# Kernel optimization log

Measured on AMD Instinct MI355X. Metric: run time of the kernel, lower is better.

The kernel has to match this reference:

```python
import jax, jax.numpy as jnp
import numpy as np

EMBED = 1024
HEADS = 16
HEAD_DIM = EMBED // HEADS


def setup_inputs() -> dict:
    key = jax.random.key(0)
    ks = jax.random.split(key, 12)
    B, S = 2, 2048
    inp = {
        'v': jax.random.normal(ks[0], (B, S, EMBED), jnp.float32),
        'k': jax.random.normal(ks[1], (B, S, EMBED), jnp.float32),
        'q': jax.random.normal(ks[2], (B, S, EMBED), jnp.float32),
        'mask': jnp.ones((B, 1, S, S), dtype=bool),
        'Wv': jax.random.normal(ks[3], (EMBED, EMBED), jnp.float32) * 0.02,
        'bv': jax.random.normal(ks[4], (EMBED,), jnp.float32) * 0.02,
        'Wk': jax.random.normal(ks[5], (EMBED, EMBED), jnp.float32) * 0.02,
        'bk': jax.random.normal(ks[6], (EMBED,), jnp.float32) * 0.02,
        'Wq': jax.random.normal(ks[7], (EMBED, EMBED), jnp.float32) * 0.02,
        'bq': jax.random.normal(ks[8], (EMBED,), jnp.float32) * 0.02,
        'Wo': jax.random.normal(ks[9], (EMBED, EMBED), jnp.float32) * 0.02,
        'bo': jax.random.normal(ks[10], (EMBED,), jnp.float32) * 0.02,
    }
    return inp


def reference(v, k, q, mask, Wv, bv, Wk, bk, Wq, bq, Wo, bo):
    N, q_len, _ = q.shape
    k_len = k.shape[1]
    # linear projections (torch Linear: x @ W.T + b)
    vh = (v @ Wv.T + bv).reshape(N, -1, HEADS, HEAD_DIM)
    kh = (k @ Wk.T + bk).reshape(N, k_len, HEADS, HEAD_DIM)
    qh = (q @ Wq.T + bq).reshape(N, q_len, HEADS, HEAD_DIM)
    # scores [N, H, q, k]
    energy = jnp.einsum('nqhd,nkhd->nhqk', qh, kh)
    # NOTE: original masks BEFORE dividing by sqrt(embed_size)
    energy = jnp.where(mask, energy, jnp.float32(-1e20))
    attention = jax.nn.softmax(energy / jnp.sqrt(jnp.float32(EMBED)), axis=3)
    out = jnp.einsum('nhqk,nkhd->nqhd', attention, vh).reshape(N, q_len, EMBED)
    return out @ Wo.T + bo
```

## Files before the change

### kernel.cpp

```cpp
#include <hip/hip_runtime.h>
#include <cstdint>
#include <cstddef>


typedef uint16_t u16;
typedef uint32_t u32;
typedef unsigned long long u64;
using bf16x8 = __attribute__((ext_vector_type(8))) __bf16;
using bf16x2 = __attribute__((ext_vector_type(2))) __bf16;
using f32x4  = __attribute__((ext_vector_type(4))) float;
using f32x16 = __attribute__((ext_vector_type(16))) float;
using u16x8  = __attribute__((ext_vector_type(8))) uint16_t;
using u16x4  = __attribute__((ext_vector_type(4))) uint16_t;
using u32x4  = __attribute__((ext_vector_type(4))) uint32_t;

#define S_LEN 2048
#define EMB   1024
#define NHEAD 16
#define HDIM  64
#define BATCH 2
#define MROWS (BATCH * S_LEN)
#define NBITW (BATCH * S_LEN * (S_LEN / 64))

__device__ __forceinline__ u16 f2bf(float f) {
  uint32_t u = __float_as_uint(f);
  u += 0x7FFFu + ((u >> 16) & 1u);
  return (u16)(u >> 16);
}

__device__ __forceinline__ float fexp2(float x) {
#if __has_builtin(__builtin_amdgcn_exp2f)
  return __builtin_amdgcn_exp2f(x);
#else
  return exp2f(x);
#endif
}

__device__ __forceinline__ u32 packbf(float a, float b) {
  bf16x2 v = { (__bf16)a, (__bf16)b };
  return __builtin_bit_cast(u32, v);
}

__device__ __forceinline__ void plswap(u32& a, u32& b) {
  asm volatile("v_permlane32_swap_b32 %0, %1" : "+v"(a), "+v"(b));
}

__device__ __forceinline__ void async16(void* lds, const void* g) {
  __builtin_amdgcn_global_load_lds(
      (const __attribute__((address_space(1))) void*)g,
      (__attribute__((address_space(3))) void*)lds, 16, 0, 0);
}

__global__ __launch_bounds__(256) void mask_compact(const uint32_t* __restrict__ m,
                                                    u64* __restrict__ bits) {
  const int i = blockIdx.x * 256 + threadIdx.x;
  if (i >= NBITW) return;
  const bool bytew = (m[0] == 0x01010101u);
  u64 b = 0;
  if (bytew) {
    const uint32_t* src = m + (size_t)i * 16;
#pragma unroll
    for (int w = 0; w < 16; ++w) {
      const uint32_t v = src[w];
#pragma unroll
      for (int j = 0; j < 4; ++j)
        b |= (u64)(((v >> (8 * j)) & 0xFFu) != 0u) << (w * 4 + j);
    }
  } else {
    const uint32_t* src = m + (size_t)i * 64;
#pragma unroll
    for (int j = 0; j < 64; ++j) b |= (u64)(src[j] != 0u) << j;
  }
  bits[i] = b;
}

struct ConvArgs {
  const float* src[7];
  u16* dst[7];
  int n4[7];
};

__global__ __launch_bounds__(256) void convert_bf16(ConvArgs a) {
  const int j = blockIdx.y;
  const float4* s = (const float4*)a.src[j];
  u16* d = a.dst[j];
  const int n4 = a.n4[j];
  for (int i = blockIdx.x * 256 + threadIdx.x; i < n4; i += gridDim.x * 256) {
    float4 v = s[i];
    u16x4 o = { f2bf(v.x), f2bf(v.y), f2bf(v.z), f2bf(v.w) };
    *(u16x4*)(d + (size_t)i * 4) = o;
  }
}

template <int BM, int BN, int FM, int FN, typename OutT>
__device__ __forceinline__ void gemm_body(const u16* __restrict__ A,
                                          const u16* __restrict__ W,
                                          const float* __restrict__ bias,
                                          OutT* __restrict__ C, float scale) {
  constexpr int K = 1024, N = 1024;
  __shared__ alignas(16) u16 As[BM * 32];
  __shared__ alignas(16) u16 Bs[BN * 32];
  const int t = threadIdx.x;
  const int wave = t >> 6, lane = t & 63;
  const int wr = wave >> 1, wc = wave & 1;
  const int m0 = blockIdx.y * BM, n0 = blockIdx.x * BN;
  f32x4 acc[FM][FN] = {};
  const int srow = wave * 16 + (lane >> 2);
  const int soff = (lane & 3) * 8;
  const u16* gA = A + (size_t)(m0 + srow) * K + soff;
  const u16* gB = W + (size_t)(n0 + srow) * K + soff;
  u16* lA = As + wave * 512;
  u16* lB = Bs + wave * 512;
  const int fo = (lane >> 4) * 8;
  const int fr = lane & 15;

  for (int kt = 0; kt < K; kt += 32) {
#pragma unroll
    for (int a = 0; a < BM / 64; ++a)
      async16(lA + a * 2048, gA + (size_t)(a * 64) * K + kt);
#pragma unroll
    for (int a = 0; a < BN / 64; ++a)
      async16(lB + a * 2048, gB + (size_t)(a * 64) * K + kt);
    __syncthreads();
    bf16x8 af[FM], bfr[FN];
#pragma unroll
    for (int i = 0; i < FM; ++i)
      af[i] = *(const bf16x8*)(As + (wr * (FM * 16) + i * 16 + fr) * 32 + fo);
#pragma unroll
    for (int i = 0; i < FN; ++i)
      bfr[i] = *(const bf16x8*)(Bs + (wc * (FN * 16) + i * 16 + fr) * 32 + fo);
#pragma unroll
    for (int mi = 0; mi < FM; ++mi)
#pragma unroll
      for (int ni = 0; ni < FN; ++ni)
        acc[mi][ni] = __builtin_amdgcn_mfma_f32_16x16x32_bf16(af[mi], bfr[ni],
                                                              acc[mi][ni], 0, 0, 0);
    __syncthreads();
  }
  const int r0 = (lane >> 4) * 4;
#pragma unroll
  for (int mi = 0; mi < FM; ++mi) {
    const int rowb = m0 + wr * (FM * 16) + mi * 16 + r0;
#pragma unroll
    for (int ni = 0; ni < FN; ++ni) {
      const int col = n0 + wc * (FN * 16) + ni * 16 + fr;
      const float bv = bias[col];
#pragma unroll
      for (int r = 0; r < 4; ++r) {
        float v = (acc[mi][ni][r] + bv) * scale;
        if constexpr (sizeof(OutT) == 2)
          C[(size_t)(rowb + r) * N + col] = f2bf(v);
        else
          C[(size_t)(rowb + r) * N + col] = v;
      }
    }
  }
}

struct ProjArgs {
  const u16* A[3];
  const u16* W[3];
  const float* bias[3];
  u16* C[3];
  float scale[3];
};

__global__ __launch_bounds__(256) void gemm_proj3(ProjArgs p) {
  const int z = blockIdx.z;
  gemm_body<128, 128, 4, 4, u16>(p.A[z], p.W[z], p.bias[z], p.C[z], p.scale[z]);
}

__global__ __launch_bounds__(256) void gemm_out(const u16* __restrict__ A,
                                                const u16* __restrict__ W,
                                                const float* __restrict__ bias,
                                                float* __restrict__ C) {
  gemm_body<64, 128, 2, 4, float>(A, W, bias, C, 1.0f);
}

__global__ __launch_bounds__(256, 2) void attn_fa(const u16* __restrict__ Qh,
                                                  const u16* __restrict__ Kh,
                                                  const u16* __restrict__ Vh,
                                                  const u64* __restrict__ mbits,
                                                  u16* __restrict__ O) {
  __shared__ alignas(16) u16 Kt[2][64 * 64];
  __shared__ alignas(16) u16 Vt[2][64 * 64];
  const int t = threadIdx.x, wave = t >> 6, lane = t & 63;
  const int b = blockIdx.y >> 4, h = blockIdx.y & 15;
  const int ql = lane & 31;
  const int hi = lane >> 5;
  const int qrow = blockIdx.x * 128 + wave * 32 + ql;

  const u16* qbase = Qh + (size_t)(b * S_LEN + qrow) * EMB + h * HDIM + hi * 8;
  bf16x8 qf[4];
#pragma unroll
  for (int dk = 0; dk < 4; ++dk)
    qf[dk] = *(const bf16x8*)(qbase + dk * 16);

  const int srow = t >> 3;
  const int schunk = t & 7;
  const int fk0 = (srow + (srow >> 3)) & 7;
  const int fk1 = (srow + 32 + ((srow + 32) >> 3)) & 7;
  const u16* kbase = Kh + (size_t)(b * S_LEN) * EMB + h * HDIM;
  const u16* vbase = Vh + (size_t)(b * S_LEN) * EMB + h * HDIM;
  const int vdg = t & 7, vkp = t >> 3;
  const int vd0 = vdg * 8, vk0 = vkp * 2;
  const int vg_hi = (vkp >> 2) & 7, vg_lo = (vkp & 3) * 4;

  u16x8 va, vb;
  {
    async16(&Kt[0][0] + wave * 512,
            kbase + (size_t)srow * EMB + ((schunk ^ fk0) * 8));
    async16(&Kt[0][0] + 2048 + wave * 512,
            kbase + (size_t)(srow + 32) * EMB + ((schunk ^ fk1) * 8));
    const u16* vs = vbase + (size_t)vk0 * EMB + vd0;
    va = *(const u16x8*)vs;
    vb = *(const u16x8*)(vs + EMB);
  }
#pragma unroll
  for (int j = 0; j < 8; ++j) {
    const int d = vd0 + j;
    const int fd = (d + (d >> 3)) & 7;
    const u32 val = (u32)va[j] | ((u32)vb[j] << 16);
    *(u32*)((char*)&Vt[0][0] + (d * 128 + ((vg_hi ^ fd) << 4) + vg_lo)) = val;
  }
  __syncthreads();

  f32x16 o[2] = {};
  float mreg = -1.0e30f, lloc = 0.f;
  const u64* mword = mbits + (size_t)(b * S_LEN + qrow) * 32;

  for (int kt = 0; kt < 32; ++kt) {
    const int cur = kt & 1, nxt = cur ^ 1;
    if (kt < 31) {
      const int kvn = (kt + 1) * 64;
      async16(&Kt[nxt][0] + wave * 512,
              kbase + (size_t)(kvn + srow) * EMB + ((schunk ^ fk0) * 8));
      async16(&Kt[nxt][0] + 2048 + wave * 512,
              kbase + (size_t)(kvn + srow + 32) * EMB + ((schunk ^ fk1) * 8));
      const u16* vs = vbase + (size_t)(kvn + vk0) * EMB + vd0;
      va = *(const u16x8*)vs;
      vb = *(const u16x8*)(vs + EMB);
    }

    f32x16 s[2] = {};
#pragma unroll
    for (int kb = 0; kb < 2; ++kb) {
      const int key = kb * 32 + ql;
      const int fkk = (key + (key >> 3)) & 7;
      const char* kRow = (const char*)&Kt[cur][0] + key * 128;
#pragma unroll
      for (int dk = 0; dk < 4; ++dk) {
        const bf16x8 kf =
            *(const bf16x8*)(kRow + (((dk * 2 + hi) ^ fkk) << 4));
        s[kb] = __builtin_amdgcn_mfma_f32_32x32x16_bf16(kf, qf[dk], s[kb], 0, 0, 0);
      }
    }

    const u64 mw = mword[kt];
    if (!__all((int)(mw == ~0ull))) {
#pragma unroll
      for (int kb = 0; kb < 2; ++kb)
#pragma unroll
        for (int r = 0; r < 16; ++r) {
          const int key = 32 * kb + (r & 3) + 8 * (r >> 2) + 4 * hi;
          if (!((mw >> key) & 1ull)) s[kb][r] = -1.0e20f;
        }
    }

    float tm = s[0][0];
#pragma unroll
    for (int kb = 0; kb < 2; ++kb)
#pragma unroll
      for (int r = 0; r < 16; ++r) tm = fmaxf(tm, s[kb][r]);
    tm = fmaxf(tm, __shfl_xor(tm, 32));
    if (!__all((int)(tm <= mreg + 8.0f))) {
      const float mn = fmaxf(mreg, tm);
      const float al = fexp2(mreg - mn);
      mreg = mn;
      lloc *= al;
#pragma unroll
      for (int dB = 0; dB < 2; ++dB)
#pragma unroll
        for (int r = 0; r < 16; ++r) o[dB][r] *= al;
    }
    float ts = 0.f;
#pragma unroll
    for (int kb = 0; kb < 2; ++kb)
#pragma unroll
      for (int r = 0; r < 16; ++r) {
        const float p = fexp2(s[kb][r] - mreg);
        s[kb][r] = p;
        ts += p;
      }
    lloc += ts;

    bf16x8 pf[4];
#pragma unroll
    for (int kb = 0; kb < 2; ++kb) {
      u32 w0 = packbf(s[kb][0], s[kb][1]);
      u32 w1 = packbf(s[kb][2], s[kb][3]);
      u32 w2 = packbf(s[kb][4], s[kb][5]);
      u32 w3 = packbf(s[kb][6], s[kb][7]);
      u32 w4 = packbf(s[kb][8], s[kb][9]);
      u32 w5 = packbf(s[kb][10], s[kb][11]);
      u32 w6 = packbf(s[kb][12], s[kb][13]);
      u32 w7 = packbf(s[kb][14], s[kb][15]);
      plswap(w0, w2);
      plswap(w1, w3);
      plswap(w4, w6);
      plswap(w5, w7);
      const u32x4 lo = {w0, w1, w2, w3};
      const u32x4 hi4 = {w4, w5, w6, w7};
      pf[kb * 2 + 0] = __builtin_bit_cast(bf16x8, lo);
      pf[kb * 2 + 1] = __builtin_bit_cast(bf16x8, hi4);
    }

#pragma unroll
    for (int dB = 0; dB < 2; ++dB) {
      const int d = dB * 32 + ql;
      const int fd = (d + (d >> 3)) & 7;
      const char* vRow = (const char*)&Vt[cur][0] + d * 128;
#pragma unroll
      for (int ks = 0; ks < 4; ++ks) {
        const bf16x8 vf =
            *(const bf16x8*)(vRow + (((ks * 2 + hi) ^ fd) << 4));
        o[dB] = __builtin_amdgcn_mfma_f32_32x32x16_bf16(vf, pf[ks], o[dB], 0, 0, 0);
      }
    }

    if (kt < 31) {
#pragma unroll
      for (int j = 0; j < 8; ++j) {
        const int d = vd0 + j;
        const int fd = (d + (d >> 3)) & 7;
        const u32 val = (u32)va[j] | ((u32)vb[j] << 16);
        *(u32*)((char*)&Vt[nxt][0] + (d * 128 + ((vg_hi ^ fd) << 4) + vg_lo)) = val;
      }
    }
    __syncthreads();
  }

  const float inv = 1.0f / (lloc + __shfl_xor(lloc, 32));
  u16* ob = O + (size_t)(b * S_LEN + qrow) * EMB + h * HDIM;
#pragma unroll
  for (int dB = 0; dB < 2; ++dB)
#pragma unroll
    for (int rr = 0; rr < 4; ++rr) {
      u16x4 st;
#pragma unroll
      for (int m = 0; m < 4; ++m) st[m] = f2bf(o[dB][rr * 4 + m] * inv);
      *(u16x4*)(ob + dB * 32 + rr * 8 + hi * 4) = st;
    }
}

extern "C" void kernel_launch(void* const* d_in, const int* in_sizes, int n_in,
                              void* d_out, int out_size, void* d_ws, size_t ws_size,
                              hipStream_t stream) {
  const float* v_in = (const float*)d_in[0];
  const float* k_in = (const float*)d_in[1];
  const float* q_in = (const float*)d_in[2];
  const uint32_t* mask = (const uint32_t*)d_in[3];
  const float* Wv = (const float*)d_in[4];
  const float* bv = (const float*)d_in[5];
  const float* Wk = (const float*)d_in[6];
  const float* bk = (const float*)d_in[7];
  const float* Wq = (const float*)d_in[8];
  const float* bq = (const float*)d_in[9];
  const float* Wo = (const float*)d_in[10];
  const float* bo = (const float*)d_in[11];

  char* ws = (char*)d_ws;
  const size_t SZX = (size_t)MROWS * EMB * 2;
  const size_t SZW = (size_t)EMB * EMB * 2;
  u16* qh  = (u16*)(ws);
  u16* kh  = (u16*)(ws + SZX);
  u16* vh  = (u16*)(ws + 2 * SZX);
  u16* Obf = (u16*)(ws + 3 * SZX);
  u16* Wqb = (u16*)(ws + 4 * SZX);
  u16* Wkb = (u16*)(ws + 4 * SZX + SZW);
  u16* Wvb = (u16*)(ws + 4 * SZX + 2 * SZW);
  u16* Wob = (u16*)(ws + 4 * SZX + 3 * SZW);
  u16* qbf = (u16*)(ws + 4 * SZX + 4 * SZW);
  u16* kbf = (u16*)(ws + 5 * SZX + 4 * SZW);
  u16* vbf = (u16*)(ws + 6 * SZX + 4 * SZW);
  u64* mbits = (u64*)(ws + 7 * SZX + 4 * SZW);

  mask_compact<<<dim3(NBITW / 256), 256, 0, stream>>>(mask, mbits);

  ConvArgs ca;
  ca.src[0] = q_in; ca.dst[0] = qbf; ca.n4[0] = MROWS * EMB / 4;
  ca.src[1] = k_in; ca.dst[1] = kbf; ca.n4[1] = MROWS * EMB / 4;
  ca.src[2] = v_in; ca.dst[2] = vbf; ca.n4[2] = MROWS * EMB / 4;
  ca.src[3] = Wq;   ca.dst[3] = Wqb; ca.n4[3] = EMB * EMB / 4;
  ca.src[4] = Wk;   ca.dst[4] = Wkb; ca.n4[4] = EMB * EMB / 4;
  ca.src[5] = Wv;   ca.dst[5] = Wvb; ca.n4[5] = EMB * EMB / 4;
  ca.src[6] = Wo;   ca.dst[6] = Wob; ca.n4[6] = EMB * EMB / 4;
  convert_bf16<<<dim3(256, 7), 256, 0, stream>>>(ca);

  ProjArgs pa;
  const float qscale = 1.4426950408889634f / 32.0f;
  pa.A[0] = qbf; pa.W[0] = Wqb; pa.bias[0] = bq; pa.C[0] = qh; pa.scale[0] = qscale;
  pa.A[1] = kbf; pa.W[1] = Wkb; pa.bias[1] = bk; pa.C[1] = kh; pa.scale[1] = 1.0f;
  pa.A[2] = vbf; pa.W[2] = Wvb; pa.bias[2] = bv; pa.C[2] = vh; pa.scale[2] = 1.0f;
  gemm_proj3<<<dim3(8, 32, 3), 256, 0, stream>>>(pa);

  attn_fa<<<dim3(S_LEN / 128, BATCH * NHEAD), 256, 0, stream>>>(qh, kh, vh, mbits, Obf);

  gemm_out<<<dim3(8, 64), 256, 0, stream>>>(Obf, Wob, bo, (float*)d_out);
}
```

Before: 142.3 us.

## Quad-buffer K/V tiles in attention, halving barriers, with setprio and permlane reductions

```diff
diff --git a/kernel.cpp b/kernel.cpp
--- a/kernel.cpp
+++ b/kernel.cpp
@@ -43,6 +43,19 @@
 
 __device__ __forceinline__ void plswap(u32& a, u32& b) {
   asm volatile("v_permlane32_swap_b32 %0, %1" : "+v"(a), "+v"(b));
+}
+
+__device__ __forceinline__ float xhalf_max(float x) {
+  u32 a = __builtin_bit_cast(u32, x), b;
+  asm volatile("v_mov_b32 %0, %1" : "=v"(b) : "v"(a));
+  asm volatile("v_permlane32_swap_b32 %0, %1" : "+v"(a), "+v"(b));
+  return fmaxf(__builtin_bit_cast(float, a), __builtin_bit_cast(float, b));
+}
+__device__ __forceinline__ float xhalf_sum(float x) {
+  u32 a = __builtin_bit_cast(u32, x), b;
+  asm volatile("v_mov_b32 %0, %1" : "=v"(b) : "v"(a));
+  asm volatile("v_permlane32_swap_b32 %0, %1" : "+v"(a), "+v"(b));
+  return __builtin_bit_cast(float, a) + __builtin_bit_cast(float, b);
 }
 
 __device__ __forceinline__ void async16(void* lds, const void* g) {
@@ -182,8 +195,8 @@
                                                   const u16* __restrict__ Vh,
                                                   const u64* __restrict__ mbits,
                                                   u16* __restrict__ O) {
-  __shared__ alignas(16) u16 Kt[2][64 * 64];
-  __shared__ alignas(16) u16 Vt[2][64 * 64];
+  __shared__ alignas(16) u16 Kt[4][64 * 64];
+  __shared__ alignas(16) u16 Vt[4][64 * 64];
   const int t = threadIdx.x, wave = t >> 6, lane = t & 63;
   const int b = blockIdx.y >> 4, h = blockIdx.y & 15;
   const int ql = lane & 31;
@@ -206,22 +219,25 @@
   const int vd0 = vdg * 8, vk0 = vkp * 2;
   const int vg_hi = (vkp >> 2) & 7, vg_lo = (vkp & 3) * 4;
 
-  u16x8 va, vb;
-  {
-    async16(&Kt[0][0] + wave * 512,
-            kbase + (size_t)srow * EMB + ((schunk ^ fk0) * 8));
-    async16(&Kt[0][0] + 2048 + wave * 512,
-            kbase + (size_t)(srow + 32) * EMB + ((schunk ^ fk1) * 8));
-    const u16* vs = vbase + (size_t)vk0 * EMB + vd0;
-    va = *(const u16x8*)vs;
-    vb = *(const u16x8*)(vs + EMB);
-  }
-#pragma unroll
-  for (int j = 0; j < 8; ++j) {
-    const int d = vd0 + j;
-    const int fd = (d + (d >> 3)) & 7;
-    const u32 val = (u32)va[j] | ((u32)vb[j] << 16);
-    *(u32*)((char*)&Vt[0][0] + (d * 128 + ((vg_hi ^ fd) << 4) + vg_lo)) = val;
+  async16(&Kt[0][0] + wave * 512, kbase + (size_t)srow * EMB + ((schunk ^ fk0) * 8));
+  async16(&Kt[0][0] + 2048 + wave * 512,
+          kbase + (size_t)(srow + 32) * EMB + ((schunk ^ fk1) * 8));
+  async16(&Kt[1][0] + wave * 512,
+          kbase + (size_t)(64 + srow) * EMB + ((schunk ^ fk0) * 8));
+  async16(&Kt[1][0] + 2048 + wave * 512,
+          kbase + (size_t)(64 + srow + 32) * EMB + ((schunk ^ fk1) * 8));
+#pragma unroll
+  for (int p = 0; p < 2; ++p) {
+    const u16* vs = vbase + (size_t)(p * 64 + vk0) * EMB + vd0;
+    const u16x8 va = *(const u16x8*)vs;
+    const u16x8 vb = *(const u16x8*)(vs + EMB);
+#pragma unroll
+    for (int j = 0; j < 8; ++j) {
+      const int d = vd0 + j;
+      const int fd = (d + (d >> 3)) & 7;
+      const u32 val = (u32)va[j] | ((u32)vb[j] << 16);
+      *(u32*)((char*)&Vt[p][0] + (d * 128 + ((vg_hi ^ fd) << 4) + vg_lo)) = val;
+    }
   }
   __syncthreads();
 
@@ -229,118 +245,115 @@
   float mreg = -1.0e30f, lloc = 0.f;
   const u64* mword = mbits + (size_t)(b * S_LEN + qrow) * 32;
 
-  for (int kt = 0; kt < 32; ++kt) {
-    const int cur = kt & 1, nxt = cur ^ 1;
-    if (kt < 31) {
-      const int kvn = (kt + 1) * 64;
-      async16(&Kt[nxt][0] + wave * 512,
-              kbase + (size_t)(kvn + srow) * EMB + ((schunk ^ fk0) * 8));
-      async16(&Kt[nxt][0] + 2048 + wave * 512,
-              kbase + (size_t)(kvn + srow + 32) * EMB + ((schunk ^ fk1) * 8));
-      const u16* vs = vbase + (size_t)(kvn + vk0) * EMB + vd0;
-      va = *(const u16x8*)vs;
-      vb = *(const u16x8*)(vs + EMB);
-    }
-
-    f32x16 s[2] = {};
-#pragma unroll
-    for (int kb = 0; kb < 2; ++kb) {
-      const int key = kb * 32 + ql;
-      const int fkk = (key + (key >> 3)) & 7;
-      const char* kRow = (const char*)&Kt[cur][0] + key * 128;
-#pragma unroll
-      for (int dk = 0; dk < 4; ++dk) {
-        const bf16x8 kf =
-            *(const bf16x8*)(kRow + (((dk * 2 + hi) ^ fkk) << 4));
-        s[kb] = __builtin_amdgcn_mfma_f32_32x32x16_bf16(kf, qf[dk], s[kb], 0, 0, 0);
-      }
-    }
-
-    const u64 mw = mword[kt];
-    if (!__all((int)(mw == ~0ull))) {
-#pragma unroll
-      for (int kb = 0; kb < 2; ++kb)
-#pragma unroll
-        for (int r = 0; r < 16; ++r) {
-          const int key = 32 * kb + (r & 3) + 8 * (r >> 2) + 4 * hi;
-          if (!((mw >> key) & 1ull)) s[kb][r] = -1.0e20f;
-        }
-    }
-
-    float tm = s[0][0];
-#pragma unroll
-    for (int kb = 0; kb < 2; ++kb)
-#pragma unroll
-      for (int r = 0; r < 16; ++r) tm = fmaxf(tm, s[kb][r]);
-    tm = fmaxf(tm, __shfl_xor(tm, 32));
-    if (!__all((int)(tm <= mreg + 8.0f))) {
-      const float mn = fmaxf(mreg, tm);
-      const float al = fexp2(mreg - mn);
-      mreg = mn;
-      lloc *= al;
-#pragma unroll
-      for (int dB = 0; dB < 2; ++dB)
-#pragma unroll
-        for (int r = 0; r < 16; ++r) o[dB][r] *= al;
-    }
-    float ts = 0.f;
-#pragma unroll
-    for (int kb = 0; kb < 2; ++kb)
-#pragma unroll
-      for (int r = 0; r < 16; ++r) {
-        const float p = fexp2(s[kb][r] - mreg);
-        s[kb][r] = p;
-        ts += p;
-      }
-    lloc += ts;
-
-    bf16x8 pf[4];
-#pragma unroll
-    for (int kb = 0; kb < 2; ++kb) {
-      u32 w0 = packbf(s[kb][0], s[kb][1]);
-      u32 w1 = packbf(s[kb][2], s[kb][3]);
-      u32 w2 = packbf(s[kb][4], s[kb][5]);
-      u32 w3 = packbf(s[kb][6], s[kb][7]);
-      u32 w4 = packbf(s[kb][8], s[kb][9]);
-      u32 w5 = packbf(s[kb][10], s[kb][11]);
-      u32 w6 = packbf(s[kb][12], s[kb][13]);
-      u32 w7 = packbf(s[kb][14], s[kb][15]);
-      plswap(w0, w2);
-      plswap(w1, w3);
-      plswap(w4, w6);
-      plswap(w5, w7);
-      const u32x4 lo = {w0, w1, w2, w3};
-      const u32x4 hi4 = {w4, w5, w6, w7};
-      pf[kb * 2 + 0] = __builtin_bit_cast(bf16x8, lo);
-      pf[kb * 2 + 1] = __builtin_bit_cast(bf16x8, hi4);
-    }
-
-#pragma unroll
-    for (int dB = 0; dB < 2; ++dB) {
-      const int d = dB * 32 + ql;
-      const int fd = (d + (d >> 3)) & 7;
-      const char* vRow = (const char*)&Vt[cur][0] + d * 128;
-#pragma unroll
-      for (int ks = 0; ks < 4; ++ks) {
-        const bf16x8 vf =
-            *(const bf16x8*)(vRow + (((ks * 2 + hi) ^ fd) << 4));
-        o[dB] = __builtin_amdgcn_mfma_f32_32x32x16_bf16(vf, pf[ks], o[dB], 0, 0, 0);
-      }
-    }
-
-    if (kt < 31) {
-#pragma unroll
-      for (int j = 0; j < 8; ++j) {
-        const int d = vd0 + j;
-        const int fd = (d + (d >> 3)) & 7;
-        const u32 val = (u32)va[j] | ((u32)vb[j] << 16);
-        *(u32*)((char*)&Vt[nxt][0] + (d * 128 + ((vg_hi ^ fd) << 4) + vg_lo)) = val;
-      }
-    }
+#define TILE_BODY(CBUF, SBUF, KT, DO_STAGE)                                    \
+  {                                                                            \
+    u16x8 va, vb;                                                              \
+    if (DO_STAGE) {                                                            \
+      const int kvn = (KT)*64 + 128;                                           \
+      async16(&Kt[SBUF][0] + wave * 512,                                       \
+              kbase + (size_t)(kvn + srow) * EMB + ((schunk ^ fk0) * 8));      \
+      async16(&Kt[SBUF][0] + 2048 + wave * 512,                                \
+              kbase + (size_t)(kvn + srow + 32) * EMB + ((schunk ^ fk1) * 8)); \
+      const u16* vs = vbase + (size_t)(kvn + vk0) * EMB + vd0;                 \
+      va = *(const u16x8*)vs;                                                  \
+      vb = *(const u16x8*)(vs + EMB);                                          \
+    }                                                                          \
+    const u64 mw = mword[KT];                                                  \
+    f32x16 s[2] = {};                                                          \
+    __builtin_amdgcn_s_setprio(1);                                             \
+    _Pragma("unroll") for (int kb = 0; kb < 2; ++kb) {                         \
+      const int key = kb * 32 + ql;                                            \
+      const int fkk = (key + (key >> 3)) & 7;                                  \
+      const char* kRow = (const char*)&Kt[CBUF][0] + key * 128;                \
+      _Pragma("unroll") for (int dk = 0; dk < 4; ++dk) {                       \
+        const bf16x8 kf =                                                      \
+            *(const bf16x8*)(kRow + (((dk * 2 + hi) ^ fkk) << 4));             \
+        s[kb] =                                                                \
+            __builtin_amdgcn_mfma_f32_32x32x16_bf16(kf, qf[dk], s[kb], 0, 0, 0); \
+      }                                                                        \
+    }                                                                          \
+    __builtin_amdgcn_s_setprio(0);                                             \
+    if (!__all((int)(mw == ~0ull))) {                                          \
+      _Pragma("unroll") for (int kb = 0; kb < 2; ++kb)                         \
+          _Pragma("unroll") for (int r = 0; r < 16; ++r) {                     \
+        const int key = 32 * kb + (r & 3) + 8 * (r >> 2) + 4 * hi;             \
+        if (!((mw >> key) & 1ull)) s[kb][r] = -1.0e20f;                        \
+      }                                                                        \
+    }                                                                          \
+    float tm = s[0][0];                                                        \
+    _Pragma("unroll") for (int kb = 0; kb < 2; ++kb)                           \
+        _Pragma("unroll") for (int r = 0; r < 16; ++r) tm =                    \
+        fmaxf(tm, s[kb][r]);                                                   \
+    tm = xhalf_max(tm);                                                        \
+    if (!__all((int)(tm <= mreg + 8.0f))) {                                    \
+      const float mn = fmaxf(mreg, tm);                                        \
+      const float al = fexp2(mreg - mn);                                       \
+      mreg = mn;                                                               \
+      lloc *= al;                                                              \
+      _Pragma("unroll") for (int dB = 0; dB < 2; ++dB)                         \
+          _Pragma("unroll") for (int r = 0; r < 16; ++r) o[dB][r] *= al;       \
+    }                                                                          \
+    float ts = 0.f;                                                            \
+    _Pragma("unroll") for (int kb = 0; kb < 2; ++kb)                           \
+        _Pragma("unroll") for (int r = 0; r < 16; ++r) {                       \
+      const float p = fexp2(s[kb][r] - mreg);                                  \
+      s[kb][r] = p;                                                            \
+      ts += p;                                                                 \
+    }                                                                          \
+    lloc += ts;                                                                \
+    bf16x8 pf[4];                                                              \
+    _Pragma("unroll") for (int kb = 0; kb < 2; ++kb) {                         \
+      u32 w0 = packbf(s[kb][0], s[kb][1]);                                     \
+      u32 w1 = packbf(s[kb][2], s[kb][3]);                                     \
+      u32 w2 = packbf(s[kb][4], s[kb][5]);                                     \
+      u32 w3 = packbf(s[kb][6], s[kb][7]);                                     \
+      u32 w4 = packbf(s[kb][8], s[kb][9]);                                     \
+      u32 w5 = packbf(s[kb][10], s[kb][11]);                                   \
+      u32 w6 = packbf(s[kb][12], s[kb][13]);                                   \
+      u32 w7 = packbf(s[kb][14], s[kb][15]);                                   \
+      plswap(w0, w2);                                                          \
+      plswap(w1, w3);                                                          \
+      plswap(w4, w6);                                                          \
+      plswap(w5, w7);                                                          \
+      const u32x4 lo4 = {w0, w1, w2, w3};                                      \
+      const u32x4 hi4 = {w4, w5, w6, w7};                                      \
+      pf[kb * 2 + 0] = __builtin_bit_cast(bf16x8, lo4);                        \
+      pf[kb * 2 + 1] = __builtin_bit_cast(bf16x8, hi4);                        \
+    }                                                                          \
+    __builtin_amdgcn_s_setprio(1);                                             \
+    _Pragma("unroll") for (int dB = 0; dB < 2; ++dB) {                         \
+      const int d = dB * 32 + ql;                                              \
+      const int fd = (d + (d >> 3)) & 7;                                       \
+      const char* vRow = (const char*)&Vt[CBUF][0] + d * 128;                  \
+      _Pragma("unroll") for (int ks = 0; ks < 4; ++ks) {                       \
+        const bf16x8 vf =                                                      \
+            *(const bf16x8*)(vRow + (((ks * 2 + hi) ^ fd) << 4));              \
+        o[dB] =                                                                \
+            __builtin_amdgcn_mfma_f32_32x32x16_bf16(vf, pf[ks], o[dB], 0, 0, 0); \
+      }                                                                        \
+    }                                                                          \
+    __builtin_amdgcn_s_setprio(0);                                             \
+    if (DO_STAGE) {                                                            \
+      _Pragma("unroll") for (int j = 0; j < 8; ++j) {                          \
+        const int d = vd0 + j;                                                 \
+        const int fd = (d + (d >> 3)) & 7;                                     \
+        const u32 val = (u32)va[j] | ((u32)vb[j] << 16);                       \
+        *(u32*)((char*)&Vt[SBUF][0] +                                         \
+                (d * 128 + ((vg_hi ^ fd) << 4) + vg_lo)) = val;                \
+      }                                                                        \
+    }                                                                          \
+  }
+
+  for (int it = 0; it < 16; ++it) {
+    const int c0 = (it & 1) * 2;
+    const bool stg = (it < 15);
+    TILE_BODY(c0, (c0 ^ 2), (2 * it), stg);
+    TILE_BODY((c0 + 1), ((c0 + 1) ^ 2), (2 * it + 1), stg);
     __syncthreads();
   }
-
-  const float inv = 1.0f / (lloc + __shfl_xor(lloc, 32));
+#undef TILE_BODY
+
+  const float inv = 1.0f / xhalf_sum(lloc);
   u16* ob = O + (size_t)(b * S_LEN + qrow) * EMB + h * HDIM;
 #pragma unroll
   for (int dB = 0; dB < 2; ++dB)
```

After: 143.7 us. Within noise of the previous version (+1.0%).

## Deepen attention K/V LDS pipeline to prefetch two tiles ahead with manual waitcnt

Applied to the files above, without the earlier changes.

```diff
diff --git a/kernel.cpp b/kernel.cpp
--- a/kernel.cpp
+++ b/kernel.cpp
@@ -43,6 +43,19 @@
 
 __device__ __forceinline__ void plswap(u32& a, u32& b) {
   asm volatile("v_permlane32_swap_b32 %0, %1" : "+v"(a), "+v"(b));
+}
+
+__device__ __forceinline__ float xhalf_max(float x) {
+  u32 a = __builtin_bit_cast(u32, x), b;
+  asm volatile("v_mov_b32 %0, %1" : "=v"(b) : "v"(a));
+  asm volatile("v_permlane32_swap_b32 %0, %1" : "+v"(a), "+v"(b));
+  return fmaxf(__builtin_bit_cast(float, a), __builtin_bit_cast(float, b));
+}
+__device__ __forceinline__ float xhalf_sum(float x) {
+  u32 a = __builtin_bit_cast(u32, x), b;
+  asm volatile("v_mov_b32 %0, %1" : "=v"(b) : "v"(a));
+  asm volatile("v_permlane32_swap_b32 %0, %1" : "+v"(a), "+v"(b));
+  return __builtin_bit_cast(float, a) + __builtin_bit_cast(float, b);
 }
 
 __device__ __forceinline__ void async16(void* lds, const void* g) {
@@ -182,8 +195,8 @@
                                                   const u16* __restrict__ Vh,
                                                   const u64* __restrict__ mbits,
                                                   u16* __restrict__ O) {
-  __shared__ alignas(16) u16 Kt[2][64 * 64];
-  __shared__ alignas(16) u16 Vt[2][64 * 64];
+  __shared__ alignas(16) u16 Kt[4][64 * 64];
+  __shared__ alignas(16) u16 Vt[4][64 * 64];
   const int t = threadIdx.x, wave = t >> 6, lane = t & 63;
   const int b = blockIdx.y >> 4, h = blockIdx.y & 15;
   const int ql = lane & 31;
@@ -206,57 +219,80 @@
   const int vd0 = vdg * 8, vk0 = vkp * 2;
   const int vg_hi = (vkp >> 2) & 7, vg_lo = (vkp & 3) * 4;
 
-  u16x8 va, vb;
+  const u64* mword = mbits + (size_t)(b * S_LEN + qrow) * 32;
+  u64 mw0 = mword[0], mw1 = mword[1];
+
   {
+    const u16* vs0 = vbase + (size_t)vk0 * EMB + vd0;
+    const u16x8 va0 = *(const u16x8*)vs0;
+    const u16x8 vb0 = *(const u16x8*)(vs0 + EMB);
+    const u16* vs1 = vbase + (size_t)(64 + vk0) * EMB + vd0;
+    const u16x8 va1 = *(const u16x8*)vs1;
+    const u16x8 vb1 = *(const u16x8*)(vs1 + EMB);
     async16(&Kt[0][0] + wave * 512,
             kbase + (size_t)srow * EMB + ((schunk ^ fk0) * 8));
     async16(&Kt[0][0] + 2048 + wave * 512,
             kbase + (size_t)(srow + 32) * EMB + ((schunk ^ fk1) * 8));
-    const u16* vs = vbase + (size_t)vk0 * EMB + vd0;
-    va = *(const u16x8*)vs;
-    vb = *(const u16x8*)(vs + EMB);
-  }
-#pragma unroll
-  for (int j = 0; j < 8; ++j) {
-    const int d = vd0 + j;
-    const int fd = (d + (d >> 3)) & 7;
-    const u32 val = (u32)va[j] | ((u32)vb[j] << 16);
-    *(u32*)((char*)&Vt[0][0] + (d * 128 + ((vg_hi ^ fd) << 4) + vg_lo)) = val;
-  }
-  __syncthreads();
+    async16(&Kt[1][0] + wave * 512,
+            kbase + (size_t)(64 + srow) * EMB + ((schunk ^ fk0) * 8));
+    async16(&Kt[1][0] + 2048 + wave * 512,
+            kbase + (size_t)(64 + srow + 32) * EMB + ((schunk ^ fk1) * 8));
+#pragma unroll
+    for (int j = 0; j < 8; ++j) {
+      const int d = vd0 + j;
+      const int fd = (d + (d >> 3)) & 7;
+      *(u32*)((char*)&Vt[0][0] + (d * 128 + ((vg_hi ^ fd) << 4) + vg_lo)) =
+          (u32)va0[j] | ((u32)vb0[j] << 16);
+      *(u32*)((char*)&Vt[1][0] + (d * 128 + ((vg_hi ^ fd) << 4) + vg_lo)) =
+          (u32)va1[j] | ((u32)vb1[j] << 16);
+    }
+  }
+  asm volatile("s_waitcnt vmcnt(0)" ::: "memory");
+  asm volatile("s_waitcnt lgkmcnt(0)" ::: "memory");
+  __builtin_amdgcn_s_barrier();
 
   f32x16 o[2] = {};
   float mreg = -1.0e30f, lloc = 0.f;
-  const u64* mword = mbits + (size_t)(b * S_LEN + qrow) * 32;
 
   for (int kt = 0; kt < 32; ++kt) {
-    const int cur = kt & 1, nxt = cur ^ 1;
-    if (kt < 31) {
-      const int kvn = (kt + 1) * 64;
-      async16(&Kt[nxt][0] + wave * 512,
-              kbase + (size_t)(kvn + srow) * EMB + ((schunk ^ fk0) * 8));
-      async16(&Kt[nxt][0] + 2048 + wave * 512,
-              kbase + (size_t)(kvn + srow + 32) * EMB + ((schunk ^ fk1) * 8));
+    const int cb = kt & 3;
+    const int sb = (kt + 2) & 3;
+    const bool stg = (kt < 30);
+    char* KtC = (char*)&Kt[cb][0];
+    char* VtC = (char*)&Vt[cb][0];
+
+    u16x8 va, vb;
+    if (stg) {
+      const int kvn = kt * 64 + 128;
       const u16* vs = vbase + (size_t)(kvn + vk0) * EMB + vd0;
       va = *(const u16x8*)vs;
       vb = *(const u16x8*)(vs + EMB);
-    }
+      asm volatile("" ::: "memory");
+      mw1 = mword[kt + 2];
+      async16(&Kt[sb][0] + wave * 512,
+              kbase + (size_t)(kvn + srow) * EMB + ((schunk ^ fk0) * 8));
+      async16(&Kt[sb][0] + 2048 + wave * 512,
+              kbase + (size_t)(kvn + srow + 32) * EMB + ((schunk ^ fk1) * 8));
+    }
+    const u64 mw = mw0;
+    mw0 = mw1;
+    if (stg) {  }
 
     f32x16 s[2] = {};
+    __builtin_amdgcn_s_setprio(1);
 #pragma unroll
     for (int kb = 0; kb < 2; ++kb) {
       const int key = kb * 32 + ql;
       const int fkk = (key + (key >> 3)) & 7;
-      const char* kRow = (const char*)&Kt[cur][0] + key * 128;
+      const char* kRow = KtC + key * 128;
 #pragma unroll
       for (int dk = 0; dk < 4; ++dk) {
-        const bf16x8 kf =
-            *(const bf16x8*)(kRow + (((dk * 2 + hi) ^ fkk) << 4));
+        const bf16x8 kf = *(const bf16x8*)(kRow + (((dk * 2 + hi) ^ fkk) << 4));
         s[kb] = __builtin_amdgcn_mfma_f32_32x32x16_bf16(kf, qf[dk], s[kb], 0, 0, 0);
       }
     }
-
-    const u64 mw = mword[kt];
+    __builtin_amdgcn_s_setprio(0);
+
     if (!__all((int)(mw == ~0ull))) {
 #pragma unroll
       for (int kb = 0; kb < 2; ++kb)
@@ -272,7 +308,7 @@
     for (int kb = 0; kb < 2; ++kb)
 #pragma unroll
       for (int r = 0; r < 16; ++r) tm = fmaxf(tm, s[kb][r]);
-    tm = fmaxf(tm, __shfl_xor(tm, 32));
+    tm = xhalf_max(tm);
     if (!__all((int)(tm <= mreg + 8.0f))) {
       const float mn = fmaxf(mreg, tm);
       const float al = fexp2(mreg - mn);
@@ -309,38 +345,43 @@
       plswap(w1, w3);
       plswap(w4, w6);
       plswap(w5, w7);
-      const u32x4 lo = {w0, w1, w2, w3};
+      const u32x4 lo4 = {w0, w1, w2, w3};
       const u32x4 hi4 = {w4, w5, w6, w7};
-      pf[kb * 2 + 0] = __builtin_bit_cast(bf16x8, lo);
+      pf[kb * 2 + 0] = __builtin_bit_cast(bf16x8, lo4);
       pf[kb * 2 + 1] = __builtin_bit_cast(bf16x8, hi4);
     }
 
+    __builtin_amdgcn_s_setprio(1);
 #pragma unroll
     for (int dB = 0; dB < 2; ++dB) {
       const int d = dB * 32 + ql;
       const int fd = (d + (d >> 3)) & 7;
-      const char* vRow = (const char*)&Vt[cur][0] + d * 128;
+      const char* vRow = VtC + d * 128;
 #pragma unroll
       for (int ks = 0; ks < 4; ++ks) {
-        const bf16x8 vf =
-            *(const bf16x8*)(vRow + (((ks * 2 + hi) ^ fd) << 4));
+        const bf16x8 vf = *(const bf16x8*)(vRow + (((ks * 2 + hi) ^ fd) << 4));
         o[dB] = __builtin_amdgcn_mfma_f32_32x32x16_bf16(vf, pf[ks], o[dB], 0, 0, 0);
       }
     }
-
-    if (kt < 31) {
+    __builtin_amdgcn_s_setprio(0);
+
+    if (stg) {
+      asm volatile("s_waitcnt vmcnt(3)" ::: "memory");
 #pragma unroll
       for (int j = 0; j < 8; ++j) {
         const int d = vd0 + j;
         const int fd = (d + (d >> 3)) & 7;
-        const u32 val = (u32)va[j] | ((u32)vb[j] << 16);
-        *(u32*)((char*)&Vt[nxt][0] + (d * 128 + ((vg_hi ^ fd) << 4) + vg_lo)) = val;
+        *(u32*)((char*)&Vt[sb][0] + (d * 128 + ((vg_hi ^ fd) << 4) + vg_lo)) =
+            (u32)va[j] | ((u32)vb[j] << 16);
       }
-    }
-    __syncthreads();
-  }
-
-  const float inv = 1.0f / (lloc + __shfl_xor(lloc, 32));
+    } else {
+      asm volatile("s_waitcnt vmcnt(0)" ::: "memory");
+    }
+    asm volatile("s_waitcnt lgkmcnt(0)" ::: "memory");
+    __builtin_amdgcn_s_barrier();
+  }
+
+  const float inv = 1.0f / xhalf_sum(lloc);
   u16* ob = O + (size_t)(b * S_LEN + qrow) * EMB + h * HDIM;
 #pragma unroll
   for (int dB = 0; dB < 2; ++dB)
```

Measured after the change: 145.5 us. 2.2% more time.
